# Performance work log

Measured on AMD Instinct MI355X. Metric: run time of the kernel, lower is better.

The kernel has to match this reference:

```python
import jax, jax.numpy as jnp
import numpy as np

B = 16384          # batch size
NUM_NEG = 4
N = 1 + NUM_NEG    # items per row (pos + negs)
D = 128            # embedding_dim
F = 4              # num_factors
FS = D // F        # factor_size = 32
TD = 384           # bert_text_dim
NU = 100000        # num_users
NI = 100000        # num_items
HID = 150          # text MLP hidden
M = 2              # num_modalities


def _linear_init(k, fan_out, fan_in):
    bound = 1.0 / np.sqrt(fan_in)
    return jax.random.uniform(k, (fan_out, fan_in), jnp.float32, -bound, bound)


def setup_inputs() -> dict:
    key = jax.random.key(0)
    ks = jax.random.split(key, 12)
    batch = jax.random.randint(ks[0], (B, 1 + N), 0, NU)          # col0=user, cols1..5=items
    text = jax.random.normal(ks[1], (B, N, TD), dtype=jnp.float32)
    user_table = jax.random.normal(ks[2], (NU, D), dtype=jnp.float32)
    item_table = jax.random.normal(ks[3], (NI, D), dtype=jnp.float32)
    w1 = _linear_init(ks[4], HID, TD)
    b1 = jax.random.uniform(ks[5], (HID,), jnp.float32, -1/np.sqrt(TD), 1/np.sqrt(TD))
    w2 = _linear_init(ks[6], D, HID)
    b2 = jax.random.uniform(ks[7], (D,), jnp.float32, -1/np.sqrt(HID), 1/np.sqrt(HID))
    # per-factor attention MLPs, stacked over the F factors (all same size here)
    aw1 = jax.random.uniform(ks[8], (F, M, 3 * FS), jnp.float32, -1/np.sqrt(3*FS), 1/np.sqrt(3*FS))
    ab1 = jax.random.uniform(ks[9], (F, M), jnp.float32, -1/np.sqrt(3*FS), 1/np.sqrt(3*FS))
    aw2 = jax.random.uniform(ks[10], (F, M, M), jnp.float32, -1/np.sqrt(M), 1/np.sqrt(M))
    return dict(batch=batch, text=text, user_table=user_table, item_table=item_table,
                w1=w1, b1=b1, w2=w2, b2=b2, aw1=aw1, ab1=ab1, aw2=aw2)


def _leaky_relu(x):
    return jnp.where(x > 0, x, 0.01 * x)


def reference(batch, text, user_table, item_table, w1, b1, w2, b2, aw1, ab1, aw2):
    # text MLP: Linear -> LeakyReLU -> Linear -> LeakyReLU
    te = _leaky_relu(_leaky_relu(text @ w1.T + b1) @ w2.T + b2)   # [B,N,D]

    users = batch[:, 0]
    items = batch[:, 1:]
    u = user_table[users]                                          # [B,D]
    ie = item_table[items]                                         # [B,N,D]

    # split into F factors of size FS (vectorized over factor dim)
    uf = jnp.broadcast_to(u[:, None, :], ie.shape).reshape(B, N, F, FS)
    itf = ie.reshape(B, N, F, FS)
    tf = te.reshape(B, N, F, FS)

    cat = jnp.concatenate([uf, itf, tf], axis=-1)                  # [B,N,F,3*FS]
    nrm = jnp.linalg.norm(cat, axis=-1, keepdims=True)
    cat = cat / jnp.maximum(nrm, 1e-12)                            # F.normalize(dim=-1)

    h = jnp.tanh(jnp.einsum('bnfk,fmk->bnfm', cat, aw1) + ab1)     # [B,N,F,M]
    logits = jnp.einsum('bnfm,fom->bnfo', h, aw2)                  # [B,N,F,M]
    # torch nn.Softmax() with dim=None on a 3D tensor -> softmax over dim 0 (batch)
    attn = jax.nn.softmax(logits, axis=0)

    r_ui = attn[..., 0] * jax.nn.softplus(jnp.sum(uf * itf, axis=-1))  # [B,N,F]
    r_ut = attn[..., 1] * jax.nn.softplus(jnp.sum(uf * tf, axis=-1))   # [B,N,F]
    ratings = jnp.sum(r_ui + r_ut, axis=-1)                        # [B,N], sum over factors
    return ratings
```

## Files before the change

### kernel.cpp

```cpp
#include <hip/hip_runtime.h>
#include <hip/hip_bf16.h>

#define TDIM 384
#define HID 150
#define DD 128
#define ROWS 81920
#define RT 64

typedef __attribute__((ext_vector_type(8))) short short8;
typedef __attribute__((ext_vector_type(4))) float f32x4;

#define SMEM_BYTES 41984

__device__ __forceinline__ float lrelu(float x) { return x > 0.f ? x : 0.01f * x; }
__device__ __forceinline__ float softplusf(float x) {
    return fmaxf(x, 0.f) + log1pf(expf(-fabsf(x)));
}

__device__ __forceinline__ short8 pack8(const float4 a, const float4 b) {
    union { short8 s; __hip_bfloat16 h[8]; } u;
    u.h[0] = __float2bfloat16(a.x); u.h[1] = __float2bfloat16(a.y);
    u.h[2] = __float2bfloat16(a.z); u.h[3] = __float2bfloat16(a.w);
    u.h[4] = __float2bfloat16(b.x); u.h[5] = __float2bfloat16(b.y);
    u.h[6] = __float2bfloat16(b.z); u.h[7] = __float2bfloat16(b.w);
    return u.s;
}

__global__ __launch_bounds__(256, 3)
void fused_main(const int* __restrict__ batch,
                const float* __restrict__ text,
                const float* __restrict__ user_table,
                const float* __restrict__ item_table,
                const float* __restrict__ w1,
                const float* __restrict__ b1,
                const float* __restrict__ w2,
                const float* __restrict__ b2,
                const float* __restrict__ aw1,
                const float* __restrict__ ab1,
                const float* __restrict__ aw2,
                float* __restrict__ expp,
                float* __restrict__ Sglob)
{
    __shared__ __align__(16) unsigned char smem[SMEM_BYTES];
    __shared__ float S_lds[40];
    __hip_bfloat16* Hs = (__hip_bfloat16*)(smem);
    float*          Ts = (float*)(smem);

    const int t    = threadIdx.x;
    const int r0   = blockIdx.x * RT;
    const int lane = t & 63;
    const int wv   = t >> 6;
    const int m16  = lane & 15;
    const int quad = lane >> 4;
    const int wr   = (wv & 1) * 32;
    const int wc   = (wv >> 1) * 80;
    const int wc2  = (wv >> 1) * 64;

    const int srow = t >> 2;
    const int sko  = (t & 3) * 8;
    const bool hasx = (t < 128);

    const int p3row = t >> 2;
    const int p3f   = t & 3;
    const int gr    = r0 + p3row;
    const int bb    = gr / 5;
    const int nn    = gr - bb * 5;
    const int uid   = batch[bb * 6];
    const int iid   = batch[bb * 6 + 1 + nn];

    if (t < 40) S_lds[t] = 0.f;

    f32x4 acc1[2][5];
#pragma unroll
    for (int i = 0; i < 2; ++i)
#pragma unroll
        for (int j = 0; j < 5; ++j) acc1[i][j] = (f32x4){0.f, 0.f, 0.f, 0.f};

    float4 pa0, pa1;
    float4 pw[3][2];

    auto loadA = [&](int kt) {
        const float* p = &text[(size_t)(r0 + srow) * TDIM + kt * 32 + sko];
        pa0 = *(const float4*)p;
        pa1 = *(const float4*)(p + 4);
    };
    auto loadW1 = [&](int kt) {
#pragma unroll
        for (int h = 0; h < 3; ++h) {
            if (h == 2 && !hasx) continue;
            const int row = srow + 64 * h;
            if (row < HID) {
                const float* p = &w1[(size_t)row * TDIM + kt * 32 + sko];
                pw[h][0] = *(const float4*)p;
                pw[h][1] = *(const float4*)(p + 4);
            } else {
                pw[h][0] = make_float4(0.f, 0.f, 0.f, 0.f);
                pw[h][1] = make_float4(0.f, 0.f, 0.f, 0.f);
            }
        }
    };
    auto store1 = [&](int p) {
        __hip_bfloat16* As  = (__hip_bfloat16*)(smem + p * 5120);
        __hip_bfloat16* Ws1 = (__hip_bfloat16*)(smem + 10240 + p * 12800);
        *(short8*)&As[srow * 40 + sko] = pack8(pa0, pa1);
#pragma unroll
        for (int h = 0; h < 3; ++h) {
            if (h == 2 && !hasx) continue;
            *(short8*)&Ws1[(srow + 64 * h) * 40 + sko] = pack8(pw[h][0], pw[h][1]);
        }
    };

    loadA(0); loadW1(0);
    store1(0);
    __syncthreads();
    for (int kt = 0; kt < 12; ++kt) {
        if (kt < 11) { loadA(kt + 1); loadW1(kt + 1); }
        const int p = kt & 1;
        const __hip_bfloat16* As  = (const __hip_bfloat16*)(smem + p * 5120);
        const __hip_bfloat16* Ws1 = (const __hip_bfloat16*)(smem + 10240 + p * 12800);
        const short8 a0 = *(const short8*)&As[(wr + m16) * 40 + quad * 8];
        const short8 a1 = *(const short8*)&As[(wr + 16 + m16) * 40 + quad * 8];
#pragma unroll
        for (int tj = 0; tj < 5; ++tj) {
            const short8 b = *(const short8*)&Ws1[(wc + tj * 16 + m16) * 40 + quad * 8];
            acc1[0][tj] = __builtin_amdgcn_mfma_f32_16x16x32_bf16(a0, b, acc1[0][tj], 0, 0, 0);
            acc1[1][tj] = __builtin_amdgcn_mfma_f32_16x16x32_bf16(a1, b, acc1[1][tj], 0, 0, 0);
        }
        if (kt < 11) store1((kt + 1) & 1);
        __syncthreads();
    }

    float pw2[2][8];
    auto loadW2 = [&](int kt) {
        const int k0 = kt * 32;
#pragma unroll
        for (int h = 0; h < 2; ++h) {
            const int idx = t + h * 256;
            const int row = idx >> 2;
            const int ko  = (idx & 3) * 8;
            const int k   = k0 + ko;
#pragma unroll
            for (int j = 0; j < 8; ++j)
                pw2[h][j] = (k + j < HID) ? w2[(size_t)row * HID + k + j] : 0.f;
        }
    };
    auto store2 = [&](int p) {
        __hip_bfloat16* Ws2 = (__hip_bfloat16*)(smem + 21504 + p * 10240);
#pragma unroll
        for (int h = 0; h < 2; ++h) {
            const int idx = t + h * 256;
            const int row = idx >> 2;
            const int ko  = (idx & 3) * 8;
            union { short8 s; __hip_bfloat16 hb[8]; } u;
#pragma unroll
            for (int j = 0; j < 8; ++j) u.hb[j] = __float2bfloat16(pw2[h][j]);
            *(short8*)&Ws2[row * 40 + ko] = u.s;
        }
    };

    loadW2(0);

#pragma unroll
    for (int tj = 0; tj < 5; ++tj) {
        const int col = wc + tj * 16 + m16;
        const float bv = (col < HID) ? b1[col] : 0.f;
#pragma unroll
        for (int ti = 0; ti < 2; ++ti) {
#pragma unroll
            for (int r = 0; r < 4; ++r) {
                const int row = wr + ti * 16 + quad * 4 + r;
                float v = lrelu(acc1[ti][tj][r] + bv);
                if (col >= HID) v = 0.f;
                Hs[row * 168 + col] = __float2bfloat16(v);
            }
        }
    }
    store2(0);
    __syncthreads();

    const float* up = user_table + (size_t)uid * DD + p3f * 32;
    const float* ip = item_table + (size_t)iid * DD + p3f * 32;
    float4 ur[8], er[8];
#pragma unroll
    for (int q = 0; q < 8; ++q) {
        ur[q] = *(const float4*)(up + q * 4);
        er[q] = *(const float4*)(ip + q * 4);
    }

    f32x4 acc2[2][4];
#pragma unroll
    for (int i = 0; i < 2; ++i)
#pragma unroll
        for (int j = 0; j < 4; ++j) acc2[i][j] = (f32x4){0.f, 0.f, 0.f, 0.f};

#pragma unroll
    for (int kt = 0; kt < 5; ++kt) {
        if (kt < 4) loadW2(kt + 1);
        const int k0 = kt * 32;
        const __hip_bfloat16* Ws2 = (const __hip_bfloat16*)(smem + 21504 + (kt & 1) * 10240);
        const short8 a0 = *(const short8*)&Hs[(wr + m16) * 168 + k0 + quad * 8];
        const short8 a1 = *(const short8*)&Hs[(wr + 16 + m16) * 168 + k0 + quad * 8];
#pragma unroll
        for (int tj = 0; tj < 4; ++tj) {
            const short8 b = *(const short8*)&Ws2[(wc2 + tj * 16 + m16) * 40 + quad * 8];
            acc2[0][tj] = __builtin_amdgcn_mfma_f32_16x16x32_bf16(a0, b, acc2[0][tj], 0, 0, 0);
            acc2[1][tj] = __builtin_amdgcn_mfma_f32_16x16x32_bf16(a1, b, acc2[1][tj], 0, 0, 0);
        }
        if (kt < 4) store2((kt + 1) & 1);
        __syncthreads();
    }

#pragma unroll
    for (int tj = 0; tj < 4; ++tj) {
        const int col = wc2 + tj * 16 + m16;
        const float bv = b2[col];
#pragma unroll
        for (int ti = 0; ti < 2; ++ti) {
#pragma unroll
            for (int r = 0; r < 4; ++r) {
                const int row = wr + ti * 16 + quad * 4 + r;
                Ts[row * 132 + col] = lrelu(acc2[ti][tj][r] + bv);
            }
        }
    }
    __syncthreads();

    {
        const float* tp  = Ts + p3row * 132 + p3f * 32;
        const float* a1p = aw1 + p3f * 2 * 96;

        float ss = 0.f, z0 = 0.f, z1 = 0.f, sui = 0.f, sut = 0.f;
#pragma unroll
        for (int q = 0; q < 8; ++q) {
            const float4 u4 = ur[q];
            const float4 e4 = er[q];
            const float4 t4 = *(const float4*)(tp + q * 4);
            const float4 a00 = *(const float4*)(a1p + q * 4);
            const float4 a01 = *(const float4*)(a1p + 32 + q * 4);
            const float4 a02 = *(const float4*)(a1p + 64 + q * 4);
            const float4 a10 = *(const float4*)(a1p + 96 + q * 4);
            const float4 a11 = *(const float4*)(a1p + 128 + q * 4);
            const float4 a12 = *(const float4*)(a1p + 160 + q * 4);
            const float uu[4] = {u4.x, u4.y, u4.z, u4.w};
            const float ee[4] = {e4.x, e4.y, e4.z, e4.w};
            const float tt[4] = {t4.x, t4.y, t4.z, t4.w};
            const float w00[4] = {a00.x, a00.y, a00.z, a00.w};
            const float w01[4] = {a01.x, a01.y, a01.z, a01.w};
            const float w02[4] = {a02.x, a02.y, a02.z, a02.w};
            const float w10[4] = {a10.x, a10.y, a10.z, a10.w};
            const float w11[4] = {a11.x, a11.y, a11.z, a11.w};
            const float w12[4] = {a12.x, a12.y, a12.z, a12.w};
#pragma unroll
            for (int c = 0; c < 4; ++c) {
                const float u = uu[c], e = ee[c], x = tt[c];
                ss  = fmaf(u, u, ss); ss = fmaf(e, e, ss); ss = fmaf(x, x, ss);
                z0  = fmaf(u, w00[c], z0);
                z0  = fmaf(e, w01[c], z0);
                z0  = fmaf(x, w02[c], z0);
                z1  = fmaf(u, w10[c], z1);
                z1  = fmaf(e, w11[c], z1);
                z1  = fmaf(x, w12[c], z1);
                sui = fmaf(u, e, sui);
                sut = fmaf(u, x, sut);
            }
        }
        const float inv = 1.f / fmaxf(sqrtf(ss), 1e-12f);
        const float h0 = tanhf(fmaf(z0, inv, ab1[p3f * 2 + 0]));
        const float h1 = tanhf(fmaf(z1, inv, ab1[p3f * 2 + 1]));
        const float l0 = fmaf(h0, aw2[p3f * 4 + 0], h1 * aw2[p3f * 4 + 1]);
        const float l1 = fmaf(h0, aw2[p3f * 4 + 2], h1 * aw2[p3f * 4 + 3]);
        const float e0 = expf(l0), e1 = expf(l1);
        const float pui = softplusf(sui), put = softplusf(sut);
        *(float4*)&expp[((size_t)gr * 4 + p3f) * 4] = make_float4(e0, e1, pui, put);
        atomicAdd(&S_lds[nn * 8 + p3f * 2 + 0], e0);
        atomicAdd(&S_lds[nn * 8 + p3f * 2 + 1], e1);
    }
    __syncthreads();
    if (t < 40) atomicAdd(&Sglob[t * 32], S_lds[t]);
}

__global__ void finalize(const float* __restrict__ expp,
                         const float* __restrict__ Sglob,
                         float* __restrict__ out)
{
    const int gr = blockIdx.x * 256 + threadIdx.x;
    if (gr >= ROWS) return;
    const int b = gr / 5;
    const int n = gr - b * 5;
    float r = 0.f;
#pragma unroll
    for (int f = 0; f < 4; ++f) {
        const float4 v = *(const float4*)&expp[((size_t)gr * 4 + f) * 4];
        const float S0 = Sglob[(n * 8 + f * 2 + 0) * 32];
        const float S1 = Sglob[(n * 8 + f * 2 + 1) * 32];
        r += v.x / S0 * v.z + v.y / S1 * v.w;
    }
    out[gr] = r;
}

extern "C" void kernel_launch(void* const* d_in, const int* in_sizes, int n_in,
                              void* d_out, int out_size, void* d_ws, size_t ws_size,
                              hipStream_t stream)
{
    (void)in_sizes; (void)n_in; (void)out_size; (void)ws_size;
    const int*   batch      = (const int*)d_in[0];
    const float* text       = (const float*)d_in[1];
    const float* user_table = (const float*)d_in[2];
    const float* item_table = (const float*)d_in[3];
    const float* w1         = (const float*)d_in[4];
    const float* b1         = (const float*)d_in[5];
    const float* w2         = (const float*)d_in[6];
    const float* b2         = (const float*)d_in[7];
    const float* aw1        = (const float*)d_in[8];
    const float* ab1        = (const float*)d_in[9];
    const float* aw2        = (const float*)d_in[10];
    float* out = (float*)d_out;

    float* expp  = (float*)d_ws;
    float* Sglob = expp + (size_t)ROWS * 16;

    hipMemsetAsync(Sglob, 0, 40 * 32 * sizeof(float), stream);
    fused_main<<<ROWS / RT, 256, 0, stream>>>(batch, text, user_table, item_table,
                                              w1, b1, w2, b2, aw1, ab1, aw2,
                                              expp, Sglob);
    finalize<<<(ROWS + 255) / 256, 256, 0, stream>>>(expp, Sglob, out);
}
```

Baseline: 356.5 us.

## Pre-convert MLP weights to bf16 tiles and deepen text prefetch pipeline

Adds a small prep kernel that converts w1 and w2 to bf16 once per call, laid out in MFMA-tile order, so the main kernel loads ready-made short8 vectors instead of converting fp32 weights in every block. The text loads are prefetched two k-steps ahead. The w2 stage drops from a double buffer to a single buffer, which shrinks shared memory and lets occupancy rise from 3 to 4 blocks per CU. The user and item embedding loads move after the second GEMM to lower register pressure, at the cost of an extra barrier per w2 step and an extra kernel launch.

```diff
diff --git a/kernel.cpp b/kernel.cpp
--- a/kernel.cpp
+++ b/kernel.cpp
@@ -10,7 +10,7 @@
 typedef __attribute__((ext_vector_type(8))) short short8;
 typedef __attribute__((ext_vector_type(4))) float f32x4;
 
-#define SMEM_BYTES 41984
+#define SMEM_BYTES 35840
 
 __device__ __forceinline__ float lrelu(float x) { return x > 0.f ? x : 0.01f * x; }
 __device__ __forceinline__ float softplusf(float x) {
@@ -26,14 +26,40 @@
     return u.s;
 }
 
-__global__ __launch_bounds__(256, 3)
+__global__ __launch_bounds__(256)
+void prep_w(const float* __restrict__ w1, const float* __restrict__ w2,
+            short8* __restrict__ w1f, short8* __restrict__ w2f)
+{
+    const int idx = blockIdx.x * 256 + threadIdx.x;
+    union { short8 s; __hip_bfloat16 h[8]; } u;
+    if (idx < 7680) {
+        const int kt = idx / 640, c = idx % 640;
+        const int col = c >> 2, q = c & 3;
+        const int k = kt * 32 + q * 8;
+#pragma unroll
+        for (int j = 0; j < 8; ++j)
+            u.h[j] = __float2bfloat16(col < HID ? w1[(size_t)col * TDIM + k + j] : 0.f);
+        w1f[idx] = u.s;
+    } else if (idx < 10240) {
+        const int i2 = idx - 7680;
+        const int kt = i2 / 512, c = i2 % 512;
+        const int col = c >> 2, q = c & 3;
+        const int k = kt * 32 + q * 8;
+#pragma unroll
+        for (int j = 0; j < 8; ++j)
+            u.h[j] = __float2bfloat16((k + j) < HID ? w2[(size_t)col * HID + k + j] : 0.f);
+        w2f[i2] = u.s;
+    }
+}
+
+__global__ __launch_bounds__(256, 4)
 void fused_main(const int* __restrict__ batch,
                 const float* __restrict__ text,
                 const float* __restrict__ user_table,
                 const float* __restrict__ item_table,
-                const float* __restrict__ w1,
+                const short8* __restrict__ w1f,
                 const float* __restrict__ b1,
-                const float* __restrict__ w2,
+                const short8* __restrict__ w2f,
                 const float* __restrict__ b2,
                 const float* __restrict__ aw1,
                 const float* __restrict__ ab1,
@@ -76,46 +102,51 @@
 #pragma unroll
         for (int j = 0; j < 5; ++j) acc1[i][j] = (f32x4){0.f, 0.f, 0.f, 0.f};
 
-    float4 pa0, pa1;
-    float4 pw[3][2];
-
-    auto loadA = [&](int kt) {
-        const float* p = &text[(size_t)(r0 + srow) * TDIM + kt * 32 + sko];
-        pa0 = *(const float4*)p;
-        pa1 = *(const float4*)(p + 4);
-    };
-    auto loadW1 = [&](int kt) {
-#pragma unroll
-        for (int h = 0; h < 3; ++h) {
-            if (h == 2 && !hasx) continue;
-            const int row = srow + 64 * h;
-            if (row < HID) {
-                const float* p = &w1[(size_t)row * TDIM + kt * 32 + sko];
-                pw[h][0] = *(const float4*)p;
-                pw[h][1] = *(const float4*)(p + 4);
+    float4 pa0a, pa0b, pa1a, pa1b;
+    short8 wr1a, wr1b, wr1c;
+
+    const float* textp = &text[(size_t)(r0 + srow) * TDIM + sko];
+
+    pa0a = *(const float4*)(textp);
+    pa0b = *(const float4*)(textp + 4);
+    wr1a = w1f[t];
+    wr1b = w1f[t + 256];
+    if (hasx) wr1c = w1f[t + 512];
+    {
+        __hip_bfloat16* As  = (__hip_bfloat16*)(smem);
+        __hip_bfloat16* Ws1 = (__hip_bfloat16*)(smem + 10240);
+        *(short8*)&As[srow * 40 + sko] = pack8(pa0a, pa0b);
+        *(short8*)&Ws1[(t >> 2) * 40 + (t & 3) * 8] = wr1a;
+        {
+            const int c = t + 256;
+            *(short8*)&Ws1[(c >> 2) * 40 + (c & 3) * 8] = wr1b;
+        }
+        if (hasx) {
+            const int c = t + 512;
+            *(short8*)&Ws1[(c >> 2) * 40 + (c & 3) * 8] = wr1c;
+        }
+    }
+    pa1a = *(const float4*)(textp + 32);
+    pa1b = *(const float4*)(textp + 36);
+    __syncthreads();
+
+#pragma unroll
+    for (int kt = 0; kt < 12; ++kt) {
+        const int p = kt & 1;
+        if (kt < 10) {
+            if (p == 0) {
+                pa0a = *(const float4*)(textp + (kt + 2) * 32);
+                pa0b = *(const float4*)(textp + (kt + 2) * 32 + 4);
             } else {
-                pw[h][0] = make_float4(0.f, 0.f, 0.f, 0.f);
-                pw[h][1] = make_float4(0.f, 0.f, 0.f, 0.f);
-            }
-        }
-    };
-    auto store1 = [&](int p) {
-        __hip_bfloat16* As  = (__hip_bfloat16*)(smem + p * 5120);
-        __hip_bfloat16* Ws1 = (__hip_bfloat16*)(smem + 10240 + p * 12800);
-        *(short8*)&As[srow * 40 + sko] = pack8(pa0, pa1);
-#pragma unroll
-        for (int h = 0; h < 3; ++h) {
-            if (h == 2 && !hasx) continue;
-            *(short8*)&Ws1[(srow + 64 * h) * 40 + sko] = pack8(pw[h][0], pw[h][1]);
-        }
-    };
-
-    loadA(0); loadW1(0);
-    store1(0);
-    __syncthreads();
-    for (int kt = 0; kt < 12; ++kt) {
-        if (kt < 11) { loadA(kt + 1); loadW1(kt + 1); }
-        const int p = kt & 1;
+                pa1a = *(const float4*)(textp + (kt + 2) * 32);
+                pa1b = *(const float4*)(textp + (kt + 2) * 32 + 4);
+            }
+        }
+        if (kt < 11) {
+            wr1a = w1f[(kt + 1) * 640 + t];
+            wr1b = w1f[(kt + 1) * 640 + t + 256];
+            if (hasx) wr1c = w1f[(kt + 1) * 640 + t + 512];
+        }
         const __hip_bfloat16* As  = (const __hip_bfloat16*)(smem + p * 5120);
         const __hip_bfloat16* Ws1 = (const __hip_bfloat16*)(smem + 10240 + p * 12800);
         const short8 a0 = *(const short8*)&As[(wr + m16) * 40 + quad * 8];
@@ -126,39 +157,26 @@
             acc1[0][tj] = __builtin_amdgcn_mfma_f32_16x16x32_bf16(a0, b, acc1[0][tj], 0, 0, 0);
             acc1[1][tj] = __builtin_amdgcn_mfma_f32_16x16x32_bf16(a1, b, acc1[1][tj], 0, 0, 0);
         }
-        if (kt < 11) store1((kt + 1) & 1);
+        if (kt < 11) {
+            __hip_bfloat16* Asn  = (__hip_bfloat16*)(smem + (p ^ 1) * 5120);
+            __hip_bfloat16* Ws1n = (__hip_bfloat16*)(smem + 10240 + (p ^ 1) * 12800);
+            *(short8*)&Asn[srow * 40 + sko] = (p == 0) ? pack8(pa1a, pa1b)
+                                                       : pack8(pa0a, pa0b);
+            *(short8*)&Ws1n[(t >> 2) * 40 + (t & 3) * 8] = wr1a;
+            {
+                const int c = t + 256;
+                *(short8*)&Ws1n[(c >> 2) * 40 + (c & 3) * 8] = wr1b;
+            }
+            if (hasx) {
+                const int c = t + 512;
+                *(short8*)&Ws1n[(c >> 2) * 40 + (c & 3) * 8] = wr1c;
+            }
+        }
         __syncthreads();
     }
 
-    float pw2[2][8];
-    auto loadW2 = [&](int kt) {
-        const int k0 = kt * 32;
-#pragma unroll
-        for (int h = 0; h < 2; ++h) {
-            const int idx = t + h * 256;
-            const int row = idx >> 2;
-            const int ko  = (idx & 3) * 8;
-            const int k   = k0 + ko;
-#pragma unroll
-            for (int j = 0; j < 8; ++j)
-                pw2[h][j] = (k + j < HID) ? w2[(size_t)row * HID + k + j] : 0.f;
-        }
-    };
-    auto store2 = [&](int p) {
-        __hip_bfloat16* Ws2 = (__hip_bfloat16*)(smem + 21504 + p * 10240);
-#pragma unroll
-        for (int h = 0; h < 2; ++h) {
-            const int idx = t + h * 256;
-            const int row = idx >> 2;
-            const int ko  = (idx & 3) * 8;
-            union { short8 s; __hip_bfloat16 hb[8]; } u;
-#pragma unroll
-            for (int j = 0; j < 8; ++j) u.hb[j] = __float2bfloat16(pw2[h][j]);
-            *(short8*)&Ws2[row * 40 + ko] = u.s;
-        }
-    };
-
-    loadW2(0);
+    short8 wr2a = w2f[t];
+    short8 wr2b = w2f[t + 256];
 
 #pragma unroll
     for (int tj = 0; tj < 5; ++tj) {
@@ -175,18 +193,8 @@
             }
         }
     }
-    store2(0);
     __syncthreads();
 
-    const float* up = user_table + (size_t)uid * DD + p3f * 32;
-    const float* ip = item_table + (size_t)iid * DD + p3f * 32;
-    float4 ur[8], er[8];
-#pragma unroll
-    for (int q = 0; q < 8; ++q) {
-        ur[q] = *(const float4*)(up + q * 4);
-        er[q] = *(const float4*)(ip + q * 4);
-    }
-
     f32x4 acc2[2][4];
 #pragma unroll
     for (int i = 0; i < 2; ++i)
@@ -195,9 +203,19 @@
 
 #pragma unroll
     for (int kt = 0; kt < 5; ++kt) {
-        if (kt < 4) loadW2(kt + 1);
+        {
+            __hip_bfloat16* Ws2 = (__hip_bfloat16*)(smem + 21504);
+            *(short8*)&Ws2[(t >> 2) * 40 + (t & 3) * 8] = wr2a;
+            const int c = t + 256;
+            *(short8*)&Ws2[(c >> 2) * 40 + (c & 3) * 8] = wr2b;
+        }
+        __syncthreads();
+        if (kt < 4) {
+            wr2a = w2f[(kt + 1) * 512 + t];
+            wr2b = w2f[(kt + 1) * 512 + t + 256];
+        }
         const int k0 = kt * 32;
-        const __hip_bfloat16* Ws2 = (const __hip_bfloat16*)(smem + 21504 + (kt & 1) * 10240);
+        const __hip_bfloat16* Ws2 = (const __hip_bfloat16*)(smem + 21504);
         const short8 a0 = *(const short8*)&Hs[(wr + m16) * 168 + k0 + quad * 8];
         const short8 a1 = *(const short8*)&Hs[(wr + 16 + m16) * 168 + k0 + quad * 8];
 #pragma unroll
@@ -206,8 +224,16 @@
             acc2[0][tj] = __builtin_amdgcn_mfma_f32_16x16x32_bf16(a0, b, acc2[0][tj], 0, 0, 0);
             acc2[1][tj] = __builtin_amdgcn_mfma_f32_16x16x32_bf16(a1, b, acc2[1][tj], 0, 0, 0);
         }
-        if (kt < 4) store2((kt + 1) & 1);
         __syncthreads();
+    }
+
+    const float* up = user_table + (size_t)uid * DD + p3f * 32;
+    const float* ip = item_table + (size_t)iid * DD + p3f * 32;
+    float4 ur[8], er[8];
+#pragma unroll
+    for (int q = 0; q < 8; ++q) {
+        ur[q] = *(const float4*)(up + q * 4);
+        er[q] = *(const float4*)(ip + q * 4);
     }
 
 #pragma unroll
@@ -316,12 +342,16 @@
     const float* aw2        = (const float*)d_in[10];
     float* out = (float*)d_out;
 
-    float* expp  = (float*)d_ws;
-    float* Sglob = expp + (size_t)ROWS * 16;
+    char* ws = (char*)d_ws;
+    short8* w1f   = (short8*)ws;
+    short8* w2f   = (short8*)(ws + 122880);
+    float*  expp  = (float*)(ws + 163840);
+    float*  Sglob = (float*)(ws + 163840 + (size_t)ROWS * 16 * 4);
 
     hipMemsetAsync(Sglob, 0, 40 * 32 * sizeof(float), stream);
+    prep_w<<<40, 256, 0, stream>>>(w1, w2, w1f, w2f);
     fused_main<<<ROWS / RT, 256, 0, stream>>>(batch, text, user_table, item_table,
-                                              w1, b1, w2, b2, aw1, ab1, aw2,
+                                              w1f, b1, w2f, b2, aw1, ab1, aw2,
                                               expp, Sglob);
     finalize<<<(ROWS + 255) / 256, 256, 0, stream>>>(expp, Sglob, out);
 }
```

Result: faster. 344.0 us (-3.5%).
